# Optimization experiments

Measured on AMD Instinct MI355X. Metric: run time of the kernel, lower is better.

Reference implementation:

```python
import jax, jax.numpy as jnp
import numpy as np

IN_DIM = 256
OUT_DIM = 64   # per-head dim
NUM_HEADS = 8
B = 8
N = 1024


def setup_inputs() -> dict:
    key = jax.random.key(0)
    k_adj, k_h, kq, kk, kv, kbq, kbk, kbv = jax.random.split(key, 8)
    adj_matrix = jax.random.randint(k_adj, (N, N), 0, 2, dtype=jnp.int32)
    h = jax.random.normal(k_h, (B, N, IN_DIM), dtype=jnp.float32)
    s = 1.0 / np.sqrt(IN_DIM)
    Wq = jax.random.normal(kq, (IN_DIM, OUT_DIM * NUM_HEADS), dtype=jnp.float32) * s
    Wk = jax.random.normal(kk, (IN_DIM, OUT_DIM * NUM_HEADS), dtype=jnp.float32) * s
    Wv = jax.random.normal(kv, (IN_DIM, OUT_DIM * NUM_HEADS), dtype=jnp.float32) * s
    bq = jax.random.normal(kbq, (OUT_DIM * NUM_HEADS,), dtype=jnp.float32) * 0.01
    bk = jax.random.normal(kbk, (OUT_DIM * NUM_HEADS,), dtype=jnp.float32) * 0.01
    bv = jax.random.normal(kbv, (OUT_DIM * NUM_HEADS,), dtype=jnp.float32) * 0.01
    return {"adj_matrix": adj_matrix, "h": h, "Wq": Wq, "bq": bq,
            "Wk": Wk, "bk": bk, "Wv": Wv, "bv": bv}


def reference(adj_matrix, h, Wq, bq, Wk, bk, Wv, bv):
    B_, N_, _ = h.shape
    H, D = NUM_HEADS, OUT_DIM
    Qh = (h @ Wq + bq).reshape(B_, N_, H, D)
    Kh = (h @ Wk + bk).reshape(B_, N_, H, D)
    Vh = (h @ Wv + bv).reshape(B_, N_, H, D)
    scores = jnp.einsum('bnhd,bmhd->bhnm', Qh, Kh) / jnp.sqrt(jnp.float32(D))
    # adjacency mask broadcast over batch and heads (neigh_attention=True)
    scores = jnp.where(adj_matrix[None, None, :, :] == 0, -jnp.inf, scores)
    attn = jax.nn.softmax(scores, axis=-1)
    out = jnp.einsum('bhnm,bmhd->bnhd', attn, Vh)
    return out.reshape(B_, N_, H * D)
```

## Files before the change

### kernel.cpp

```cpp
#include <hip/hip_runtime.h>
#include <math.h>

#define IN_DIM 256
#define HD     512
#define NHEADS 8
#define DH     64
#define NSEQ   1024
#define BATCH  8

#define QSCALE 0.18033688011112042f

typedef unsigned short u16;
typedef unsigned int   u32;
typedef unsigned long long u64;
typedef short bf16x8 __attribute__((ext_vector_type(8)));
typedef float f32x4  __attribute__((ext_vector_type(4)));

#if __has_builtin(__builtin_amdgcn_exp2f)
#define EXP2(x) __builtin_amdgcn_exp2f(x)
#else
#define EXP2(x) __expf(0.69314718056f * (x))
#endif

static __device__ __forceinline__ u16 f2bf(float x) {
    u32 u = __builtin_bit_cast(u32, x);
    u += 0x7FFFu + ((u >> 16) & 1u);
    return (u16)(u >> 16);
}
static __device__ __forceinline__ float bf2f(u16 x) {
    return __builtin_bit_cast(float, ((u32)x) << 16);
}
static __device__ __forceinline__ u32 pk(u16 a, u16 b) {
    return (u32)a | ((u32)b << 16);
}
static __device__ __forceinline__ u32 cvtpk(float a, float b) {
    return pk(f2bf(a), f2bf(b));
}

__global__ __launch_bounds__(256)
void prep_kernel(const float* __restrict__ Wq, const float* __restrict__ Wk,
                 const float* __restrict__ Wv, const int* __restrict__ adj,
                 u16* __restrict__ Wt, u16* __restrict__ MaddT)
{
    __shared__ u32 shpool[64 * 65];
    const int bid = blockIdx.x, tid = threadIdx.x;

    if (bid < 96) {
        float* tile = (float*)shpool;
        const int wk = bid;
        const int k0 = (wk & 3) * 64, n0 = ((wk >> 2) & 7) * 64, wsel = wk >> 5;
        const float* W = (wsel == 0) ? Wq : (wsel == 1) ? Wk : Wv;
        u16* Out = Wt + (size_t)wsel * HD * IN_DIM;

        const int r = tid >> 2, c0 = (tid & 3) * 16;
#pragma unroll
        for (int j = 0; j < 16; j += 4) {
            float4 v = *(const float4*)(W + (size_t)(k0 + r) * HD + n0 + c0 + j);
            tile[r * 65 + c0 + j + 0] = v.x; tile[r * 65 + c0 + j + 1] = v.y;
            tile[r * 65 + c0 + j + 2] = v.z; tile[r * 65 + c0 + j + 3] = v.w;
        }
        __syncthreads();
        const int n = tid >> 2, ks = (tid & 3) * 16;
        u16 o[16];
#pragma unroll
        for (int j = 0; j < 16; ++j) o[j] = f2bf(tile[(ks + j) * 65 + n]);
        uint4 u0, u1;
        u0.x = pk(o[0], o[1]);   u0.y = pk(o[2], o[3]);
        u0.z = pk(o[4], o[5]);   u0.w = pk(o[6], o[7]);
        u1.x = pk(o[8], o[9]);   u1.y = pk(o[10], o[11]);
        u1.z = pk(o[12], o[13]); u1.w = pk(o[14], o[15]);
        u16* dst = Out + (size_t)(n0 + n) * IN_DIM + k0 + ks;
        *(uint4*)(dst) = u0;
        *(uint4*)(dst + 8) = u1;
    } else {
        int* tile = (int*)shpool;
        const int abid = bid - 96;
        const int tR = abid >> 4, tC = abid & 15;
        const int r = tid >> 2, cg = (tid & 3) * 16;
        const int* src = adj + (size_t)(tR * 64 + r) * NSEQ + tC * 64 + cg;
#pragma unroll
        for (int j = 0; j < 16; j += 4) {
            int4 a = *(const int4*)(src + j);
            tile[r * 65 + cg + j + 0] = a.x; tile[r * 65 + cg + j + 1] = a.y;
            tile[r * 65 + cg + j + 2] = a.z; tile[r * 65 + cg + j + 3] = a.w;
        }
        __syncthreads();
        const int kk = tid >> 2, qg = (tid & 3) * 16;
        u16 o[16];
#pragma unroll
        for (int j = 0; j < 16; ++j)
            o[j] = (tile[(qg + j) * 65 + kk] == 0) ? (u16)0xFF7F : (u16)0;
        uint4 u0, u1;
        u0.x = pk(o[0], o[1]);   u0.y = pk(o[2], o[3]);
        u0.z = pk(o[4], o[5]);   u0.w = pk(o[6], o[7]);
        u1.x = pk(o[8], o[9]);   u1.y = pk(o[10], o[11]);
        u1.z = pk(o[12], o[13]); u1.w = pk(o[14], o[15]);
        u16* dst = MaddT + (size_t)(tC * 64 + kk) * NSEQ + tR * 64 + qg;
        *(uint4*)(dst) = u0;
        *(uint4*)(dst + 8) = u1;
    }
}

__global__ __launch_bounds__(256, 2)
void qkv_gemm_kernel(const float* __restrict__ h, const u16* __restrict__ Wt,
                     const float* __restrict__ bq, const float* __restrict__ bk,
                     const float* __restrict__ bv,
                     u16* __restrict__ Qg, u16* __restrict__ Kg,
                     u16* __restrict__ Vtg)
{
    __shared__ u16 pool[128 * 64 + 3 * 64 * 64];
    u16* As = pool;
    u16* Bs = pool + 128 * 64;

    const int m0 = blockIdx.x * 128;
    const int hh = blockIdx.y;
    const int n0 = hh * 64;

    const int tid = threadIdx.x;
    const int w = tid >> 6, lane = tid & 63, l15 = lane & 15, quad = lane >> 4;
    const int sw = l15 & 7;

    f32x4 acc[3][2][4];
#pragma unroll
    for (int wh = 0; wh < 3; ++wh)
#pragma unroll
        for (int rs = 0; rs < 2; ++rs)
#pragma unroll
            for (int t = 0; t < 4; ++t) acc[wh][rs][t] = (f32x4){0.f, 0.f, 0.f, 0.f};

    const int arow = tid >> 1, acg = (tid & 1) * 4;
    const int brow = tid & 63, bgrp = tid >> 6;
    const float* srcA = h + (size_t)(m0 + arow) * IN_DIM;

    for (int kk = 0; kk < IN_DIM; kk += 64) {
        __syncthreads();
#pragma unroll
        for (int g = 0; g < 4; ++g) {
            const float* p = srcA + kk + (acg + g) * 8;
            float4 v0 = *(const float4*)(p);
            float4 v1 = *(const float4*)(p + 4);
            uint4 u;
            u.x = cvtpk(v0.x, v0.y); u.y = cvtpk(v0.z, v0.w);
            u.z = cvtpk(v1.x, v1.y); u.w = cvtpk(v1.z, v1.w);
            *(uint4*)&As[arow * 64 + (((acg + g) ^ (arow & 7)) * 8)] = u;
        }
#pragma unroll
        for (int i = 0; i < 6; ++i) {
            const int gc = bgrp * 6 + i;
            const int wh = gc >> 3, c8 = gc & 7;
            *(uint4*)&Bs[wh * 4096 + brow * 64 + ((c8 ^ (brow & 7)) * 8)] =
                *(const uint4*)(Wt + (size_t)wh * HD * IN_DIM +
                                (size_t)(n0 + brow) * IN_DIM + kk + c8 * 8);
        }
        __syncthreads();
        bf16x8 a[2][2];
#pragma unroll
        for (int rs = 0; rs < 2; ++rs) {
            const int ra = (w * 32 + rs * 16 + l15) * 64;
            a[rs][0] = *(const bf16x8*)&As[ra + ((quad ^ sw) * 8)];
            a[rs][1] = *(const bf16x8*)&As[ra + (((4 + quad) ^ sw) * 8)];
        }
#pragma unroll
        for (int t = 0; t < 4; ++t) {
            const int rb = (t * 16 + l15) * 64;
#pragma unroll
            for (int wh = 0; wh < 3; ++wh) {
                bf16x8 b0 = *(const bf16x8*)&Bs[wh * 4096 + rb + ((quad ^ sw) * 8)];
                bf16x8 b1 = *(const bf16x8*)&Bs[wh * 4096 + rb + (((4 + quad) ^ sw) * 8)];
#pragma unroll
                for (int rs = 0; rs < 2; ++rs) {
                    acc[wh][rs][t] = __builtin_amdgcn_mfma_f32_16x16x32_bf16(a[rs][0], b0, acc[wh][rs][t], 0, 0, 0);
                    acc[wh][rs][t] = __builtin_amdgcn_mfma_f32_16x16x32_bf16(a[rs][1], b1, acc[wh][rs][t], 0, 0, 0);
                }
            }
        }
    }

    for (int which = 0; which < 2; ++which) {
        u16* T = pool;
        const float* bias = (which == 0) ? bq : bk;
        u16* Out = (which == 0) ? Qg : Kg;
        const float scale = (which == 0) ? QSCALE : 1.0f;
        __syncthreads();
#pragma unroll
        for (int t = 0; t < 4; ++t) {
            const float bvv = bias[n0 + t * 16 + l15];
#pragma unroll
            for (int rs = 0; rs < 2; ++rs) {
                const int rowb = w * 32 + rs * 16 + quad * 4;
#pragma unroll
                for (int r = 0; r < 4; ++r)
                    T[(rowb + r) * 72 + t * 16 + l15] =
                        f2bf((acc[which][rs][t][r] + bvv) * scale);
            }
        }
        __syncthreads();
        const int row = tid >> 1, half = tid & 1;
        u16* dst = Out + (size_t)(m0 + row) * HD + n0 + half * 32;
        const u16* srcT = &T[row * 72 + half * 32];
#pragma unroll
        for (int i = 0; i < 4; ++i)
            *(uint4*)(dst + i * 8) = *(const uint4*)(srcT + i * 8);
    }

    {
        u16* T = pool;
        __syncthreads();
#pragma unroll
        for (int t = 0; t < 4; ++t) {
            const float bvv = bv[n0 + t * 16 + l15];
            const int trow = (t * 16 + l15) * 136;
#pragma unroll
            for (int rs = 0; rs < 2; ++rs) {
                const int base = w * 32 + rs * 16 + quad * 4;
                const int c64 = base >> 6;
                const int mloc = base & 63;
                const int cb = c64 * 64 + ((mloc & 15) * 4) + (mloc >> 4);
#pragma unroll
                for (int r = 0; r < 4; ++r)
                    T[trow + cb + 4 * r] = f2bf(acc[2][rs][t][r] + bvv);
            }
        }
        __syncthreads();
        const int b = m0 >> 10, nloc = m0 & 1023;
        const int d = tid >> 2, c = (tid & 3) * 32;
        u16* dst = Vtg + ((size_t)(b * NHEADS + hh) * DH + d) * NSEQ + nloc + c;
#pragma unroll
        for (int i = 0; i < 4; ++i)
            *(uint4*)(dst + i * 8) = *(uint4*)&T[d * 136 + c + i * 8];
    }
}

__global__ __launch_bounds__(512, 4)
void attn_kernel(const u16* __restrict__ MaddT, const u16* __restrict__ Qg,
                 const u16* __restrict__ Kg, const u16* __restrict__ Vtg,
                 float* __restrict__ out)
{
    __shared__ u16 Ks[2][64 * 64];
    __shared__ u16 Vs[2][64 * 64];
    __shared__ u16 Ps[128 * 64];

    const int tid = threadIdx.x;
    const int w = tid >> 6, lane = tid & 63, l15 = lane & 15, quad = lane >> 4;
    const int qt = blockIdx.x, bh = blockIdx.y;
    const int b = bh >> 3;
    const int n0 = qt * 128;
    const size_t rowbase = (size_t)b * NSEQ;
    const int colbase = (bh & 7) * DH;
    const int sw = l15 & 7;

    const u16* qrow = Qg + (rowbase + n0 + w * 16 + l15) * HD + colbase;
    const bf16x8 qa0 = *(const bf16x8*)(qrow + quad * 8);
    const bf16x8 qa1 = *(const bf16x8*)(qrow + 32 + quad * 8);

    const int srow = tid >> 3, c8w = tid & 7;
    const int swc = ((c8w ^ (srow & 7)) * 8);
    const u16* kgp = Kg + (rowbase + srow) * HD + colbase + c8w * 8;
    const u16* vgp = Vtg + ((size_t)bh * DH + srow) * NSEQ + c8w * 8;
    const u16* mgp = MaddT + (size_t)l15 * NSEQ + n0 + w * 16 + quad * 4;

    uint4 kG = *(const uint4*)kgp;
    uint4 vG = *(const uint4*)vgp;
    ushort4 mG[4];
#pragma unroll
    for (int t = 0; t < 4; ++t) mG[t] = *(const ushort4*)(mgp + (size_t)(t * 16) * NSEQ);

    *(uint4*)&Ks[0][srow * 64 + swc] = kG;
    *(uint4*)&Vs[0][srow * 64 + swc] = vG;
    __syncthreads();

    float lrow[4] = {0.f, 0.f, 0.f, 0.f};
    f32x4 O[4];
#pragma unroll
    for (int t = 0; t < 4; ++t) O[t] = (f32x4){0.f, 0.f, 0.f, 0.f};

    const int pwbase = (w * 16 + quad * 4) * 64;
    const int parow  = (w * 16 + l15) * 64;

    for (int ch = 0; ch < 16; ++ch) {
        const int cur = ch & 1;

        f32x4 s4[4];
#pragma unroll
        for (int t = 0; t < 4; ++t)
            s4[t] = (f32x4){bf2f(mG[t].x), bf2f(mG[t].y), bf2f(mG[t].z), bf2f(mG[t].w)};

        if (ch < 15) {
            kG = *(const uint4*)(kgp + (size_t)(ch + 1) * 64 * HD);
            vG = *(const uint4*)(vgp + (ch + 1) * 64);
#pragma unroll
            for (int t = 0; t < 4; ++t)
                mG[t] = *(const ushort4*)(mgp + ((size_t)(ch + 1) * 64 + t * 16) * NSEQ);
        }

#pragma unroll
        for (int t = 0; t < 4; ++t) {
            const int rb = (t * 16 + l15) * 64;
            bf16x8 kb0 = *(const bf16x8*)&Ks[cur][rb + ((quad ^ sw) * 8)];
            bf16x8 kb1 = *(const bf16x8*)&Ks[cur][rb + (((4 + quad) ^ sw) * 8)];
            s4[t] = __builtin_amdgcn_mfma_f32_16x16x32_bf16(qa0, kb0, s4[t], 0, 0, 0);
            s4[t] = __builtin_amdgcn_mfma_f32_16x16x32_bf16(qa1, kb1, s4[t], 0, 0, 0);
        }

        if (ch < 15) {
            *(uint4*)&Ks[1 - cur][srow * 64 + swc] = kG;
            *(uint4*)&Vs[1 - cur][srow * 64 + swc] = vG;
        }

#pragma unroll
        for (int r = 0; r < 4; ++r) {
            float p0 = EXP2(s4[0][r]);
            float p1 = EXP2(s4[1][r]);
            float p2 = EXP2(s4[2][r]);
            float p3 = EXP2(s4[3][r]);
            lrow[r] += (p0 + p1) + (p2 + p3);
            uint2 pw;
            pw.x = cvtpk(p0, p1);
            pw.y = cvtpk(p2, p3);
            const int q7 = (quad * 4 + r) & 7;
            *(uint2*)&Ps[pwbase + r * 64 + (((l15 >> 1) ^ q7) * 8) + (l15 & 1) * 4] = pw;
        }

        {
            bf16x8 pa0 = *(const bf16x8*)&Ps[parow + ((quad ^ sw) * 8)];
            bf16x8 pa1 = *(const bf16x8*)&Ps[parow + (((4 + quad) ^ sw) * 8)];
#pragma unroll
            for (int t = 0; t < 4; ++t) {
                const int rb = (t * 16 + l15) * 64;
                bf16x8 vb0 = *(const bf16x8*)&Vs[cur][rb + ((quad ^ sw) * 8)];
                bf16x8 vb1 = *(const bf16x8*)&Vs[cur][rb + (((4 + quad) ^ sw) * 8)];
                O[t] = __builtin_amdgcn_mfma_f32_16x16x32_bf16(pa0, vb0, O[t], 0, 0, 0);
                O[t] = __builtin_amdgcn_mfma_f32_16x16x32_bf16(pa1, vb1, O[t], 0, 0, 0);
            }
        }
        __syncthreads();
    }

#pragma unroll
    for (int d = 1; d < 16; d <<= 1)
#pragma unroll
        for (int r = 0; r < 4; ++r)
            lrow[r] += __shfl_xor(lrow[r], d, 64);

    float inv[4];
#pragma unroll
    for (int r = 0; r < 4; ++r) inv[r] = 1.0f / lrow[r];
#pragma unroll
    for (int t = 0; t < 4; ++t)
#pragma unroll
        for (int r = 0; r < 4; ++r)
            out[(rowbase + n0 + w * 16 + quad * 4 + r) * HD + colbase + t * 16 + l15] =
                O[t][r] * inv[r];
}

extern "C" void kernel_launch(void* const* d_in, const int* in_sizes, int n_in,
                              void* d_out, int out_size, void* d_ws, size_t ws_size,
                              hipStream_t stream) {
    const int*   adj = (const int*)d_in[0];
    const float* h   = (const float*)d_in[1];
    const float* Wq  = (const float*)d_in[2];
    const float* bq  = (const float*)d_in[3];
    const float* Wk  = (const float*)d_in[4];
    const float* bk  = (const float*)d_in[5];
    const float* Wv  = (const float*)d_in[6];
    const float* bv  = (const float*)d_in[7];
    float* outp = (float*)d_out;

    u16* Wt    = (u16*)d_ws;
    u16* Qg    = Wt + (size_t)3 * HD * IN_DIM;
    u16* Kg    = Qg + (size_t)BATCH * NSEQ * HD;
    u16* Vtg   = Kg + (size_t)BATCH * NSEQ * HD;
    u16* MaddT = Vtg + (size_t)BATCH * NSEQ * HD;

    prep_kernel<<<352, 256, 0, stream>>>(Wq, Wk, Wv, adj, Wt, MaddT);
    qkv_gemm_kernel<<<dim3(BATCH * NSEQ / 128, NHEADS), 256, 0, stream>>>(
        h, Wt, bq, bk, bv, Qg, Kg, Vtg);
    attn_kernel<<<dim3(NSEQ / 128, BATCH * NHEADS), 512, 0, stream>>>(
        MaddT, Qg, Kg, Vtg, outp);
}
```

Before: 142.8 us.

## Shrink QKV GEMM tile, store mask as fp32, reorder attention grid

The QKV projection tile drops from 128 to 64 rows per block, and the launch bound now requests four blocks per CU. The goal is more blocks in flight and fewer registers per thread. The additive adjacency mask is stored as fp32 instead of bf16, which removes the per-element conversion in the attention loop but doubles the mask traffic. The attention grid is swapped so that blocks sharing a query tile but covering different batch-heads launch together, and the bf16 pack now uses the HIP intrinsic.

```diff
diff --git a/kernel.cpp b/kernel.cpp
--- a/kernel.cpp
+++ b/kernel.cpp
@@ -1,4 +1,5 @@
 #include <hip/hip_runtime.h>
+#include <hip/hip_bf16.h>
 #include <math.h>
 
 #define IN_DIM 256
@@ -8,11 +9,11 @@
 #define NSEQ   1024
 #define BATCH  8
 
-#define QSCALE 0.18033688011112042f
+#define QSCALE  0.18033688011112042f
+#define MASKVAL -3.0e38f
 
 typedef unsigned short u16;
 typedef unsigned int   u32;
-typedef unsigned long long u64;
 typedef short bf16x8 __attribute__((ext_vector_type(8)));
 typedef float f32x4  __attribute__((ext_vector_type(4)));
 
@@ -27,20 +28,19 @@
     u += 0x7FFFu + ((u >> 16) & 1u);
     return (u16)(u >> 16);
 }
-static __device__ __forceinline__ float bf2f(u16 x) {
-    return __builtin_bit_cast(float, ((u32)x) << 16);
-}
 static __device__ __forceinline__ u32 pk(u16 a, u16 b) {
     return (u32)a | ((u32)b << 16);
 }
 static __device__ __forceinline__ u32 cvtpk(float a, float b) {
-    return pk(f2bf(a), f2bf(b));
+    __hip_bfloat162 t = __float22bfloat162_rn(make_float2(a, b));
+    u32 r; __builtin_memcpy(&r, &t, 4);
+    return r;
 }
 
 __global__ __launch_bounds__(256)
 void prep_kernel(const float* __restrict__ Wq, const float* __restrict__ Wk,
                  const float* __restrict__ Wv, const int* __restrict__ adj,
-                 u16* __restrict__ Wt, u16* __restrict__ MaddT)
+                 u16* __restrict__ Wt, float* __restrict__ MaddF)
 {
     __shared__ u32 shpool[64 * 65];
     const int bid = blockIdx.x, tid = threadIdx.x;
@@ -86,33 +86,31 @@
         }
         __syncthreads();
         const int kk = tid >> 2, qg = (tid & 3) * 16;
-        u16 o[16];
-#pragma unroll
-        for (int j = 0; j < 16; ++j)
-            o[j] = (tile[(qg + j) * 65 + kk] == 0) ? (u16)0xFF7F : (u16)0;
-        uint4 u0, u1;
-        u0.x = pk(o[0], o[1]);   u0.y = pk(o[2], o[3]);
-        u0.z = pk(o[4], o[5]);   u0.w = pk(o[6], o[7]);
-        u1.x = pk(o[8], o[9]);   u1.y = pk(o[10], o[11]);
-        u1.z = pk(o[12], o[13]); u1.w = pk(o[14], o[15]);
-        u16* dst = MaddT + (size_t)(tC * 64 + kk) * NSEQ + tR * 64 + qg;
-        *(uint4*)(dst) = u0;
-        *(uint4*)(dst + 8) = u1;
-    }
-}
-
-__global__ __launch_bounds__(256, 2)
+        float* dst = MaddF + (size_t)(tC * 64 + kk) * NSEQ + tR * 64 + qg;
+#pragma unroll
+        for (int j = 0; j < 16; j += 4) {
+            float4 o;
+            o.x = (tile[(qg + j + 0) * 65 + kk] == 0) ? MASKVAL : 0.f;
+            o.y = (tile[(qg + j + 1) * 65 + kk] == 0) ? MASKVAL : 0.f;
+            o.z = (tile[(qg + j + 2) * 65 + kk] == 0) ? MASKVAL : 0.f;
+            o.w = (tile[(qg + j + 3) * 65 + kk] == 0) ? MASKVAL : 0.f;
+            *(float4*)(dst + j) = o;
+        }
+    }
+}
+
+__global__ __launch_bounds__(256, 4)
 void qkv_gemm_kernel(const float* __restrict__ h, const u16* __restrict__ Wt,
                      const float* __restrict__ bq, const float* __restrict__ bk,
                      const float* __restrict__ bv,
                      u16* __restrict__ Qg, u16* __restrict__ Kg,
                      u16* __restrict__ Vtg)
 {
-    __shared__ u16 pool[128 * 64 + 3 * 64 * 64];
+    __shared__ u16 pool[64 * 64 + 3 * 64 * 64];
     u16* As = pool;
-    u16* Bs = pool + 128 * 64;
-
-    const int m0 = blockIdx.x * 128;
+    u16* Bs = pool + 64 * 64;
+
+    const int m0 = blockIdx.x * 64;
     const int hh = blockIdx.y;
     const int n0 = hh * 64;
 
@@ -120,22 +118,20 @@
     const int w = tid >> 6, lane = tid & 63, l15 = lane & 15, quad = lane >> 4;
     const int sw = l15 & 7;
 
-    f32x4 acc[3][2][4];
+    f32x4 acc[3][4];
 #pragma unroll
     for (int wh = 0; wh < 3; ++wh)
 #pragma unroll
-        for (int rs = 0; rs < 2; ++rs)
-#pragma unroll
-            for (int t = 0; t < 4; ++t) acc[wh][rs][t] = (f32x4){0.f, 0.f, 0.f, 0.f};
-
-    const int arow = tid >> 1, acg = (tid & 1) * 4;
+        for (int t = 0; t < 4; ++t) acc[wh][t] = (f32x4){0.f, 0.f, 0.f, 0.f};
+
+    const int arow = tid >> 2, acg = (tid & 3) * 2;
     const int brow = tid & 63, bgrp = tid >> 6;
     const float* srcA = h + (size_t)(m0 + arow) * IN_DIM;
 
     for (int kk = 0; kk < IN_DIM; kk += 64) {
         __syncthreads();
 #pragma unroll
-        for (int g = 0; g < 4; ++g) {
+        for (int g = 0; g < 2; ++g) {
             const float* p = srcA + kk + (acg + g) * 8;
             float4 v0 = *(const float4*)(p);
             float4 v1 = *(const float4*)(p + 4);
@@ -153,13 +149,9 @@
                                 (size_t)(n0 + brow) * IN_DIM + kk + c8 * 8);
         }
         __syncthreads();
-        bf16x8 a[2][2];
-#pragma unroll
-        for (int rs = 0; rs < 2; ++rs) {
-            const int ra = (w * 32 + rs * 16 + l15) * 64;
-            a[rs][0] = *(const bf16x8*)&As[ra + ((quad ^ sw) * 8)];
-            a[rs][1] = *(const bf16x8*)&As[ra + (((4 + quad) ^ sw) * 8)];
-        }
+        const int ra = (w * 16 + l15) * 64;
+        bf16x8 a0 = *(const bf16x8*)&As[ra + ((quad ^ sw) * 8)];
+        bf16x8 a1 = *(const bf16x8*)&As[ra + (((4 + quad) ^ sw) * 8)];
 #pragma unroll
         for (int t = 0; t < 4; ++t) {
             const int rb = (t * 16 + l15) * 64;
@@ -167,11 +159,8 @@
             for (int wh = 0; wh < 3; ++wh) {
                 bf16x8 b0 = *(const bf16x8*)&Bs[wh * 4096 + rb + ((quad ^ sw) * 8)];
                 bf16x8 b1 = *(const bf16x8*)&Bs[wh * 4096 + rb + (((4 + quad) ^ sw) * 8)];
-#pragma unroll
-                for (int rs = 0; rs < 2; ++rs) {
-                    acc[wh][rs][t] = __builtin_amdgcn_mfma_f32_16x16x32_bf16(a[rs][0], b0, acc[wh][rs][t], 0, 0, 0);
-                    acc[wh][rs][t] = __builtin_amdgcn_mfma_f32_16x16x32_bf16(a[rs][1], b1, acc[wh][rs][t], 0, 0, 0);
-                }
+                acc[wh][t] = __builtin_amdgcn_mfma_f32_16x16x32_bf16(a0, b0, acc[wh][t], 0, 0, 0);
+                acc[wh][t] = __builtin_amdgcn_mfma_f32_16x16x32_bf16(a1, b1, acc[wh][t], 0, 0, 0);
             }
         }
     }
@@ -185,22 +174,18 @@
 #pragma unroll
         for (int t = 0; t < 4; ++t) {
             const float bvv = bias[n0 + t * 16 + l15];
-#pragma unroll
-            for (int rs = 0; rs < 2; ++rs) {
-                const int rowb = w * 32 + rs * 16 + quad * 4;
-#pragma unroll
-                for (int r = 0; r < 4; ++r)
-                    T[(rowb + r) * 72 + t * 16 + l15] =
-                        f2bf((acc[which][rs][t][r] + bvv) * scale);
-            }
-        }
-        __syncthreads();
-        const int row = tid >> 1, half = tid & 1;
-        u16* dst = Out + (size_t)(m0 + row) * HD + n0 + half * 32;
-        const u16* srcT = &T[row * 72 + half * 32];
-#pragma unroll
-        for (int i = 0; i < 4; ++i)
-            *(uint4*)(dst + i * 8) = *(const uint4*)(srcT + i * 8);
+            const int rowb = w * 16 + quad * 4;
+#pragma unroll
+            for (int r = 0; r < 4; ++r)
+                T[(rowb + r) * 72 + t * 16 + l15] =
+                    f2bf((acc[which][t][r] + bvv) * scale);
+        }
+        __syncthreads();
+        const int row = tid >> 2, qc = (tid & 3) * 16;
+        u16* dst = Out + (size_t)(m0 + row) * HD + n0 + qc;
+        const u16* srcT = &T[row * 72 + qc];
+        *(uint4*)(dst)     = *(const uint4*)(srcT);
+        *(uint4*)(dst + 8) = *(const uint4*)(srcT + 8);
     }
 
     {
@@ -209,30 +194,22 @@
 #pragma unroll
         for (int t = 0; t < 4; ++t) {
             const float bvv = bv[n0 + t * 16 + l15];
-            const int trow = (t * 16 + l15) * 136;
-#pragma unroll
-            for (int rs = 0; rs < 2; ++rs) {
-                const int base = w * 32 + rs * 16 + quad * 4;
-                const int c64 = base >> 6;
-                const int mloc = base & 63;
-                const int cb = c64 * 64 + ((mloc & 15) * 4) + (mloc >> 4);
-#pragma unroll
-                for (int r = 0; r < 4; ++r)
-                    T[trow + cb + 4 * r] = f2bf(acc[2][rs][t][r] + bvv);
-            }
+            const int trow = (t * 16 + l15) * 72;
+#pragma unroll
+            for (int r = 0; r < 4; ++r)
+                T[trow + (quad * 4 + r) * 4 + w] = f2bf(acc[2][t][r] + bvv);
         }
         __syncthreads();
         const int b = m0 >> 10, nloc = m0 & 1023;
-        const int d = tid >> 2, c = (tid & 3) * 32;
+        const int d = tid >> 2, c = (tid & 3) * 16;
         u16* dst = Vtg + ((size_t)(b * NHEADS + hh) * DH + d) * NSEQ + nloc + c;
-#pragma unroll
-        for (int i = 0; i < 4; ++i)
-            *(uint4*)(dst + i * 8) = *(uint4*)&T[d * 136 + c + i * 8];
+        *(uint4*)(dst)     = *(uint4*)&T[d * 72 + c];
+        *(uint4*)(dst + 8) = *(uint4*)&T[d * 72 + c + 8];
     }
 }
 
 __global__ __launch_bounds__(512, 4)
-void attn_kernel(const u16* __restrict__ MaddT, const u16* __restrict__ Qg,
+void attn_kernel(const float* __restrict__ MaddF, const u16* __restrict__ Qg,
                  const u16* __restrict__ Kg, const u16* __restrict__ Vtg,
                  float* __restrict__ out)
 {
@@ -242,7 +219,7 @@
 
     const int tid = threadIdx.x;
     const int w = tid >> 6, lane = tid & 63, l15 = lane & 15, quad = lane >> 4;
-    const int qt = blockIdx.x, bh = blockIdx.y;
+    const int bh = blockIdx.x, qt = blockIdx.y;
     const int b = bh >> 3;
     const int n0 = qt * 128;
     const size_t rowbase = (size_t)b * NSEQ;
@@ -257,13 +234,13 @@
     const int swc = ((c8w ^ (srow & 7)) * 8);
     const u16* kgp = Kg + (rowbase + srow) * HD + colbase + c8w * 8;
     const u16* vgp = Vtg + ((size_t)bh * DH + srow) * NSEQ + c8w * 8;
-    const u16* mgp = MaddT + (size_t)l15 * NSEQ + n0 + w * 16 + quad * 4;
+    const float* mgp = MaddF + (size_t)l15 * NSEQ + n0 + w * 16 + quad * 4;
 
     uint4 kG = *(const uint4*)kgp;
     uint4 vG = *(const uint4*)vgp;
-    ushort4 mG[4];
-#pragma unroll
-    for (int t = 0; t < 4; ++t) mG[t] = *(const ushort4*)(mgp + (size_t)(t * 16) * NSEQ);
+    float4 mG[4];
+#pragma unroll
+    for (int t = 0; t < 4; ++t) mG[t] = *(const float4*)(mgp + (size_t)(t * 16) * NSEQ);
 
     *(uint4*)&Ks[0][srow * 64 + swc] = kG;
     *(uint4*)&Vs[0][srow * 64 + swc] = vG;
@@ -283,14 +260,14 @@
         f32x4 s4[4];
 #pragma unroll
         for (int t = 0; t < 4; ++t)
-            s4[t] = (f32x4){bf2f(mG[t].x), bf2f(mG[t].y), bf2f(mG[t].z), bf2f(mG[t].w)};
+            s4[t] = (f32x4){mG[t].x, mG[t].y, mG[t].z, mG[t].w};
 
         if (ch < 15) {
             kG = *(const uint4*)(kgp + (size_t)(ch + 1) * 64 * HD);
             vG = *(const uint4*)(vgp + (ch + 1) * 64);
 #pragma unroll
             for (int t = 0; t < 4; ++t)
-                mG[t] = *(const ushort4*)(mgp + ((size_t)(ch + 1) * 64 + t * 16) * NSEQ);
+                mG[t] = *(const float4*)(mgp + ((size_t)(ch + 1) * 64 + t * 16) * NSEQ);
         }
 
 #pragma unroll
@@ -366,15 +343,15 @@
     const float* bv  = (const float*)d_in[7];
     float* outp = (float*)d_out;
 
-    u16* Wt    = (u16*)d_ws;
-    u16* Qg    = Wt + (size_t)3 * HD * IN_DIM;
-    u16* Kg    = Qg + (size_t)BATCH * NSEQ * HD;
-    u16* Vtg   = Kg + (size_t)BATCH * NSEQ * HD;
-    u16* MaddT = Vtg + (size_t)BATCH * NSEQ * HD;
-
-    prep_kernel<<<352, 256, 0, stream>>>(Wq, Wk, Wv, adj, Wt, MaddT);
-    qkv_gemm_kernel<<<dim3(BATCH * NSEQ / 128, NHEADS), 256, 0, stream>>>(
+    u16* Wt     = (u16*)d_ws;
+    u16* Qg     = Wt + (size_t)3 * HD * IN_DIM;
+    u16* Kg     = Qg + (size_t)BATCH * NSEQ * HD;
+    u16* Vtg    = Kg + (size_t)BATCH * NSEQ * HD;
+    float* MaddF = (float*)(Vtg + (size_t)BATCH * NSEQ * HD);
+
+    prep_kernel<<<352, 256, 0, stream>>>(Wq, Wk, Wv, adj, Wt, MaddF);
+    qkv_gemm_kernel<<<dim3(BATCH * NSEQ / 64, NHEADS), 256, 0, stream>>>(
         h, Wt, bq, bk, bv, Qg, Kg, Vtg);
-    attn_kernel<<<dim3(NSEQ / 128, BATCH * NHEADS), 512, 0, stream>>>(
-        MaddT, Qg, Kg, Vtg, outp);
-}
+    attn_kernel<<<dim3(BATCH * NHEADS, NSEQ / 128), 512, 0, stream>>>(
+        MaddF, Qg, Kg, Vtg, outp);
+}
```

Result: no change. 140.9 us (-1.3%).
